# Kernel optimization log

Hardware: AMD Instinct MI355X
Metric: run time of the kernel (lower is better)

The kernel has to match this reference:

```python
import jax, jax.numpy as jnp
import numpy as np

EMBED_DIM = 512
NUM_HEADS = 8
HEAD_DIM = EMBED_DIM // NUM_HEADS
SCALE = HEAD_DIM ** -0.5


def setup_inputs() -> dict:
    key = jax.random.key(0)
    ks = jax.random.split(key, 5)
    B, N, C = 4, 2048, EMBED_DIM
    s = 0.02
    return {
        "x": jax.random.normal(ks[0], (B, N, C), jnp.float32),
        "qkv_w": jax.random.normal(ks[1], (3 * C, C), jnp.float32) * s,
        "qkv_b": jax.random.normal(ks[2], (3 * C,), jnp.float32) * s,
        "proj_w": jax.random.normal(ks[3], (C, C), jnp.float32) * s,
        "proj_b": jax.random.normal(ks[4], (C,), jnp.float32) * s,
    }


def reference(x, qkv_w, qkv_b, proj_w, proj_b):
    B, N, C = x.shape
    H, D = NUM_HEADS, HEAD_DIM
    # qkv: (B, N, 3C) -> (3, B, H, N, D)
    qkv = x @ qkv_w.T + qkv_b
    qkv = qkv.reshape(B, N, 3, H, D).transpose(2, 0, 3, 1, 4)
    q, k, v = qkv[0], qkv[1], qkv[2]
    attn = jnp.einsum("bhnd,bhmd->bhnm", q, k) * SCALE  # (B,H,N,N)
    attn = jax.nn.softmax(attn, axis=-1)
    out = jnp.einsum("bhnm,bhmd->bhnd", attn, v)  # (B,H,N,D)
    out = out.transpose(0, 2, 1, 3).reshape(B, N, C)
    return out @ proj_w.T + proj_b
```

## Files before the change

kernel.cpp:

```cpp
#include <hip/hip_runtime.h>

#define ED 512
#define NH 8
#define HD 64
#define BB 4
#define SEQ 2048
#define MTOT (BB*SEQ)

typedef float f32x4 __attribute__((ext_vector_type(4)));
typedef float f32x16 __attribute__((ext_vector_type(16)));
typedef __bf16 bf16x8 __attribute__((ext_vector_type(8)));
typedef int i32x2 __attribute__((ext_vector_type(2)));
typedef unsigned int u32x4 __attribute__((ext_vector_type(4)));

__device__ __forceinline__ unsigned short f2bf(float f) {
  unsigned int u = __float_as_uint(f);
  u += 0x7FFFu + ((u >> 16) & 1u);
  return (unsigned short)(u >> 16);
}

__device__ __forceinline__ unsigned int cvtpk(float lo, float hi) {
  unsigned int r;
  asm volatile("v_cvt_pk_bf16_f32 %0, %1, %2" : "=v"(r) : "v"(lo), "v"(hi));
  return r;
}

__device__ __forceinline__ void async16(const void* g, void* l) {
  auto gp = (const __attribute__((address_space(1))) unsigned int*)(uintptr_t)(g);
  auto lp = (__attribute__((address_space(3))) unsigned int*)(uintptr_t)(l);
  __builtin_amdgcn_global_load_lds(gp, lp, 16, 0, 0);
}

#define N4_X   1048576
#define N4_WQ  196608
#define N4_WP  65536
__global__ void cvt_all(const float* __restrict__ x,
                        const float* __restrict__ wq_in,
                        const float* __restrict__ wp_in,
                        unsigned short* __restrict__ xb,
                        unsigned short* __restrict__ wq,
                        unsigned short* __restrict__ wp) {
  int i = blockIdx.x * blockDim.x + threadIdx.x;
  const float* src; unsigned short* dst; int off;
  if (i < N4_X)              { src = x;     dst = xb; off = i; }
  else if (i < N4_X + N4_WQ) { src = wq_in; dst = wq; off = i - N4_X; }
  else                       { src = wp_in; dst = wp; off = i - (N4_X + N4_WQ); }
  float4 v = reinterpret_cast<const float4*>(src)[off];
  ushort4 o;
  o.x = f2bf(v.x); o.y = f2bf(v.y); o.z = f2bf(v.z); o.w = f2bf(v.w);
  reinterpret_cast<ushort4*>(dst)[off] = o;
}

template<int MODE, int BM, int NXB>
__global__ __launch_bounds__(256)
void gemm_bt(const unsigned short* __restrict__ A,
             const unsigned short* __restrict__ B,
             const float* __restrict__ bias,
             int M, int N, int K,
             unsigned short* __restrict__ Qo,
             unsigned short* __restrict__ Ko,
             unsigned short* __restrict__ Vo,
             float* __restrict__ Co) {
  __shared__ __align__(16) unsigned short As[2][BM * 64];
  __shared__ __align__(16) unsigned short Bs[2][128 * 64];
  const int FI = BM / 32;
  const int t = threadIdx.x;
  const int l = t & 63;
  const int w = t >> 6;
  const int lo = l & 15, hi = l >> 4;
  const int wr = w >> 1, wc = w & 1;
  const int bid = blockIdx.x;
  const int xcd = bid & 7, idx = bid >> 3;
  const int ypx = (M / BM) >> 3;
  const int m0 = (xcd * ypx + idx / NXB) * BM;
  const int n0 = (idx % NXB) * 128;

  f32x4 acc[FI][4] = {};

  auto stage = [&](int buf, int kt) {
    #pragma unroll
    for (int it = 0; it < BM / 32; ++it) {
      int c = it * 256 + t;
      int row = c >> 3, cin = c & 7;
      int sw = cin ^ (row & 7);
      async16(A + (size_t)(m0 + row) * K + kt * 64 + sw * 8, &As[buf][c * 8]);
    }
    #pragma unroll
    for (int it = 0; it < 4; ++it) {
      int c = it * 256 + t;
      int row = c >> 3, cin = c & 7;
      int sw = cin ^ (row & 7);
      async16(B + (size_t)(n0 + row) * K + kt * 64 + sw * 8, &Bs[buf][c * 8]);
    }
  };

  const int nkt = K >> 6;
  stage(0, 0);
  asm volatile("s_waitcnt vmcnt(0)" ::: "memory");
  __syncthreads();

  for (int kt = 0; kt < nkt; ++kt) {
    const int cur = kt & 1;
    if (kt + 1 < nkt) stage(cur ^ 1, kt + 1);

    __builtin_amdgcn_s_setprio(1);
    #pragma unroll
    for (int kk = 0; kk < 2; ++kk) {
      bf16x8 af[FI], bf[4];
      #pragma unroll
      for (int i = 0; i < FI; ++i) {
        int ra = wr * (BM / 2) + i * 16 + lo;
        int ch = (kk * 4 + hi) ^ (lo & 7);
        af[i] = *reinterpret_cast<const bf16x8*>(&As[cur][ra * 64 + ch * 8]);
      }
      #pragma unroll
      for (int j = 0; j < 4; ++j) {
        int rb = wc * 64 + j * 16 + lo;
        int ch = (kk * 4 + hi) ^ (lo & 7);
        bf[j] = *reinterpret_cast<const bf16x8*>(&Bs[cur][rb * 64 + ch * 8]);
      }
      #pragma unroll
      for (int i = 0; i < FI; ++i)
        #pragma unroll
        for (int j = 0; j < 4; ++j)
          acc[i][j] = __builtin_amdgcn_mfma_f32_16x16x32_bf16(af[i], bf[j], acc[i][j], 0, 0, 0);
    }
    __builtin_amdgcn_s_setprio(0);

    asm volatile("s_waitcnt vmcnt(0)" ::: "memory");
    __syncthreads();
  }

  if (MODE == 0) {
    #pragma unroll
    for (int j = 0; j < 4; ++j) {
      int gcol = n0 + wc * 64 + j * 16 + lo;
      float bv = bias[gcol];
      int which = gcol >> 9;
      int h = (gcol >> 6) & 7;
      int d = gcol & 63;
      #pragma unroll
      for (int i = 0; i < FI; ++i) {
        int rbase = m0 + wr * (BM / 2) + i * 16 + hi * 4;
        int b = rbase >> 11;
        size_t bh = (size_t)(b * NH + h);
        if (which == 2) {
          ushort4 pk;
          pk.x = f2bf(acc[i][j][0] + bv);
          pk.y = f2bf(acc[i][j][1] + bv);
          pk.z = f2bf(acc[i][j][2] + bv);
          pk.w = f2bf(acc[i][j][3] + bv);
          int seq = rbase & 2047;
          *reinterpret_cast<ushort4*>(&Vo[(bh * HD + d) * SEQ + seq]) = pk;
        } else {
          #pragma unroll
          for (int e = 0; e < 4; ++e) {
            int seq = (rbase + e) & 2047;
            float v = acc[i][j][e] + bv;
            if (which == 0)
              Qo[(bh * SEQ + seq) * HD + d] = f2bf(v * 0.18033688f);
            else
              Ko[(bh * SEQ + seq) * HD + d] = f2bf(v);
          }
        }
      }
    }
  } else {
    #pragma unroll
    for (int j = 0; j < 4; ++j) {
      int gcol = n0 + wc * 64 + j * 16 + lo;
      float bv = bias[gcol];
      #pragma unroll
      for (int i = 0; i < FI; ++i) {
        int rbase = m0 + wr * (BM / 2) + i * 16 + hi * 4;
        #pragma unroll
        for (int e = 0; e < 4; ++e)
          Co[(size_t)(rbase + e) * N + gcol] = acc[i][j][e] + bv;
      }
    }
  }
}

__global__ __launch_bounds__(512, 4)
void attn_kernel(const unsigned short* __restrict__ Q,
                 const unsigned short* __restrict__ Kk,
                 const unsigned short* __restrict__ Vt,
                 unsigned short* __restrict__ Ao) {
  __shared__ __align__(16) unsigned short smem[32768];
  auto KsP = [&](int half, int buf) { return &smem[(half * 2 + buf) * 4096]; };
  auto VsP = [&](int half, int buf) { return &smem[16384 + (half * 2 + buf) * 4096]; };
  const int t = threadIdx.x;
  const int l = t & 63;
  const int wid = t >> 6;
  const int qg = wid & 3;
  const int kvh = wid >> 2;
  const int l31 = l & 31, lh = l >> 5;
  const int bid = blockIdx.x;
  const int xcd = bid & 7, idx = bid >> 3;
  const int bh = xcd * 4 + (idx >> 4);
  const int q0 = (idx & 15) * 128;
  const int b = bh >> 3, h = bh & 7;

  bf16x8 qf[4];
  #pragma unroll
  for (int ks = 0; ks < 4; ++ks)
    qf[ks] = *reinterpret_cast<const bf16x8*>(
        &Q[((size_t)bh * SEQ + q0 + qg * 32 + l31) * HD + ks * 16 + lh * 8]);

  f32x16 o0 = {}, o1 = {}, osum = {};
  const __bf16 one1 = (__bf16)1.0f;
  const bf16x8 ones = {one1, one1, one1, one1, one1, one1, one1, one1};

  auto stage = [&](int buf, int kt) {
    const int half = t >> 8;
    const int tt = t & 255;
    const int sbase = half * 1024 + kt * 64;
    unsigned short* kd = KsP(half, buf);
    unsigned short* vd = VsP(half, buf);
    #pragma unroll
    for (int it = 0; it < 2; ++it) {
      int c = it * 256 + tt;
      int row = c >> 3, cin = c & 7;
      int sw = cin ^ (row & 7);
      async16(&Kk[((size_t)bh * SEQ + sbase + row) * HD + sw * 8], kd + c * 8);
    }
    #pragma unroll
    for (int it = 0; it < 2; ++it) {
      int c = it * 256 + tt;
      int row = c >> 3, cin = c & 7;
      int sw = cin ^ (row & 7);
      async16(&Vt[((size_t)bh * HD + row) * SEQ + sbase + sw * 8], vd + c * 8);
    }
  };

  auto tile = [&](int cur, int kt) {
    if (kt + 1 < 16) stage(cur ^ 1, kt + 1);
    const unsigned short* kp = KsP(kvh, cur);
    const unsigned short* vp = VsP(kvh, cur);

    #pragma unroll
    for (int kn = 0; kn < 2; ++kn) {
      f32x16 s = {};
      __builtin_amdgcn_s_setprio(1);
      #pragma unroll
      for (int ks = 0; ks < 4; ++ks) {
        int row = kn * 32 + l31;
        int ch = ((ks * 2 + lh) ^ (l31 & 7)) * 8;
        bf16x8 kf = *reinterpret_cast<const bf16x8*>(&kp[row * 64 + ch]);
        s = __builtin_amdgcn_mfma_f32_32x32x16_bf16(kf, qf[ks], s, 0, 0, 0);
      }
      __builtin_amdgcn_s_setprio(0);

      #pragma unroll
      for (int i = 0; i < 16; ++i) s[i] = __builtin_amdgcn_exp2f(s[i]);

      #pragma unroll
      for (int hs = 0; hs < 2; ++hs) {
        unsigned int w0 = cvtpk(s[8 * hs + 0], s[8 * hs + 1]);
        unsigned int w1 = cvtpk(s[8 * hs + 2], s[8 * hs + 3]);
        unsigned int w2 = cvtpk(s[8 * hs + 4], s[8 * hs + 5]);
        unsigned int w3 = cvtpk(s[8 * hs + 6], s[8 * hs + 7]);
        i32x2 r0 = __builtin_amdgcn_permlane32_swap((int)w0, (int)w2, false, false);
        i32x2 r1 = __builtin_amdgcn_permlane32_swap((int)w1, (int)w3, false, false);
        u32x4 fw = {(unsigned int)r0.x, (unsigned int)r1.x,
                    (unsigned int)r0.y, (unsigned int)r1.y};
        bf16x8 pf = __builtin_bit_cast(bf16x8, fw);

        int ss = kn * 2 + hs;
        int vch = ((ss * 2 + lh) ^ (l31 & 7)) * 8;
        __builtin_amdgcn_s_setprio(1);
        osum = __builtin_amdgcn_mfma_f32_32x32x16_bf16(pf, ones, osum, 0, 0, 0);
        bf16x8 vf0 = *reinterpret_cast<const bf16x8*>(&vp[l31 * 64 + vch]);
        bf16x8 vf1 = *reinterpret_cast<const bf16x8*>(&vp[(32 + l31) * 64 + vch]);
        o0 = __builtin_amdgcn_mfma_f32_32x32x16_bf16(pf, vf0, o0, 0, 0, 0);
        o1 = __builtin_amdgcn_mfma_f32_32x32x16_bf16(pf, vf1, o1, 0, 0, 0);
        __builtin_amdgcn_s_setprio(0);
      }
    }

    asm volatile("s_waitcnt vmcnt(0)" ::: "memory");
    __syncthreads();
  };

  stage(0, 0);
  asm volatile("s_waitcnt vmcnt(0)" ::: "memory");
  __syncthreads();

  for (int k2 = 0; k2 < 8; ++k2) {
    tile(0, 2 * k2);
    tile(1, 2 * k2 + 1);
  }

  float* lds = reinterpret_cast<float*>(&smem[0]);
  const int slot = qg * 64 + l;
  auto coff = [&](int c) {
    return (size_t)slot * 64 + (((c & ~7) | ((c & 7) ^ (l & 7))) << 2);
  };
  if (kvh == 1) {
    #pragma unroll
    for (int c = 0; c < 4; ++c) {
      *reinterpret_cast<f32x4*>(lds + coff(c))     = f32x4{o0[4*c], o0[4*c+1], o0[4*c+2], o0[4*c+3]};
      *reinterpret_cast<f32x4*>(lds + coff(c + 4)) = f32x4{o1[4*c], o1[4*c+1], o1[4*c+2], o1[4*c+3]};
      *reinterpret_cast<f32x4*>(lds + coff(c + 8)) = f32x4{osum[4*c], osum[4*c+1], osum[4*c+2], osum[4*c+3]};
    }
  }
  __syncthreads();
  if (kvh == 0) {
    #pragma unroll
    for (int c = 0; c < 4; ++c) {
      f32x4 a0 = *reinterpret_cast<const f32x4*>(lds + coff(c));
      f32x4 a1 = *reinterpret_cast<const f32x4*>(lds + coff(c + 4));
      f32x4 a2 = *reinterpret_cast<const f32x4*>(lds + coff(c + 8));
      #pragma unroll
      for (int e = 0; e < 4; ++e) {
        o0[4*c+e] += a0[e]; o1[4*c+e] += a1[e]; osum[4*c+e] += a2[e];
      }
    }

    #pragma unroll
    for (int r = 0; r < 16; ++r) {
      int qoff = (r & 3) + 8 * (r >> 2) + 4 * lh;
      int seq = q0 + qg * 32 + qoff;
      float inv = 1.f / osum[r];
      size_t base2 = ((size_t)b * SEQ + seq) * ED + h * HD;
      Ao[base2 + l31]      = f2bf(o0[r] * inv);
      Ao[base2 + 32 + l31] = f2bf(o1[r] * inv);
    }
  }
}

extern "C" void kernel_launch(void* const* d_in, const int* in_sizes, int n_in,
                              void* d_out, int out_size, void* d_ws, size_t ws_size,
                              hipStream_t stream) {
  const float* x      = (const float*)d_in[0];
  const float* qkv_w  = (const float*)d_in[1];
  const float* qkv_b  = (const float*)d_in[2];
  const float* proj_w = (const float*)d_in[3];
  const float* proj_b = (const float*)d_in[4];
  float* out = (float*)d_out;

  char* ws = (char*)d_ws;
  unsigned short* xb = (unsigned short*)(ws);
  unsigned short* wq = (unsigned short*)(ws + 8388608);
  unsigned short* wp = (unsigned short*)(ws + 9961472);
  unsigned short* Q  = (unsigned short*)(ws + 10485760);
  unsigned short* Kb = (unsigned short*)(ws + 18874368);
  unsigned short* Vt = (unsigned short*)(ws + 27262976);
  unsigned short* Ao = (unsigned short*)(ws + 35651584);

  cvt_all<<<(N4_X + N4_WQ + N4_WP + 255) / 256, 256, 0, stream>>>(
      x, qkv_w, proj_w, xb, wq, wp);

  gemm_bt<0, 128, 12><<<768, 256, 0, stream>>>(xb, wq, qkv_b, MTOT, 3 * ED, ED, Q, Kb, Vt, nullptr);

  attn_kernel<<<512, 512, 0, stream>>>(Q, Kb, Vt, Ao);

  gemm_bt<1, 64, 4><<<512, 256, 0, stream>>>(Ao, wp, proj_b, MTOT, ED, ED, nullptr, nullptr, nullptr, out);
}
```

Measured before the change: 82.24 us.

## Fuse fp32-to-bf16 conversion of x into the QKV GEMM A-tile staging

New measurement: 83.63 us. Within noise of the previous version (+1.7%).

```diff
diff --git a/kernel.cpp b/kernel.cpp
--- a/kernel.cpp
+++ b/kernel.cpp
@@ -31,20 +31,16 @@
   __builtin_amdgcn_global_load_lds(gp, lp, 16, 0, 0);
 }
 
-#define N4_X   1048576
 #define N4_WQ  196608
 #define N4_WP  65536
-__global__ void cvt_all(const float* __restrict__ x,
-                        const float* __restrict__ wq_in,
-                        const float* __restrict__ wp_in,
-                        unsigned short* __restrict__ xb,
-                        unsigned short* __restrict__ wq,
-                        unsigned short* __restrict__ wp) {
+__global__ void cvt_w(const float* __restrict__ wq_in,
+                      const float* __restrict__ wp_in,
+                      unsigned short* __restrict__ wq,
+                      unsigned short* __restrict__ wp) {
   int i = blockIdx.x * blockDim.x + threadIdx.x;
   const float* src; unsigned short* dst; int off;
-  if (i < N4_X)              { src = x;     dst = xb; off = i; }
-  else if (i < N4_X + N4_WQ) { src = wq_in; dst = wq; off = i - N4_X; }
-  else                       { src = wp_in; dst = wp; off = i - (N4_X + N4_WQ); }
+  if (i < N4_WQ) { src = wq_in; dst = wq; off = i; }
+  else           { src = wp_in; dst = wp; off = i - N4_WQ; }
   float4 v = reinterpret_cast<const float4*>(src)[off];
   ushort4 o;
   o.x = f2bf(v.x); o.y = f2bf(v.y); o.z = f2bf(v.z); o.w = f2bf(v.w);
@@ -53,7 +49,7 @@
 
 template<int MODE, int BM, int NXB>
 __global__ __launch_bounds__(256)
-void gemm_bt(const unsigned short* __restrict__ A,
+void gemm_bt(const void* __restrict__ Aptr,
              const unsigned short* __restrict__ B,
              const float* __restrict__ bias,
              int M, int N, int K,
@@ -75,16 +71,13 @@
   const int m0 = (xcd * ypx + idx / NXB) * BM;
   const int n0 = (idx % NXB) * 128;
 
+  const float* Af = (const float*)Aptr;
+  const unsigned short* Ab = (const unsigned short*)Aptr;
+
   f32x4 acc[FI][4] = {};
-
-  auto stage = [&](int buf, int kt) {
-    #pragma unroll
-    for (int it = 0; it < BM / 32; ++it) {
-      int c = it * 256 + t;
-      int row = c >> 3, cin = c & 7;
-      int sw = cin ^ (row & 7);
-      async16(A + (size_t)(m0 + row) * K + kt * 64 + sw * 8, &As[buf][c * 8]);
-    }
+  f32x4 alo[FI], ahi[FI];
+
+  auto stageB = [&](int buf, int kt) {
     #pragma unroll
     for (int it = 0; it < 4; ++it) {
       int c = it * 256 + t;
@@ -93,16 +86,40 @@
       async16(B + (size_t)(n0 + row) * K + kt * 64 + sw * 8, &Bs[buf][c * 8]);
     }
   };
-
-  const int nkt = K >> 6;
-  stage(0, 0);
-  asm volatile("s_waitcnt vmcnt(0)" ::: "memory");
-  __syncthreads();
-
-  for (int kt = 0; kt < nkt; ++kt) {
-    const int cur = kt & 1;
-    if (kt + 1 < nkt) stage(cur ^ 1, kt + 1);
-
+  auto stageA_async = [&](int buf, int kt) {
+    #pragma unroll
+    for (int it = 0; it < BM / 32; ++it) {
+      int c = it * 256 + t;
+      int row = c >> 3, cin = c & 7;
+      int sw = cin ^ (row & 7);
+      async16(Ab + (size_t)(m0 + row) * K + kt * 64 + sw * 8, &As[buf][c * 8]);
+    }
+  };
+  auto stageA_load = [&](int kt) {
+    #pragma unroll
+    for (int it = 0; it < BM / 32; ++it) {
+      int c = it * 256 + t;
+      int row = c >> 3, cin = c & 7;
+      int sw = cin ^ (row & 7);
+      const float* src = Af + (size_t)(m0 + row) * K + kt * 64 + sw * 8;
+      alo[it] = *reinterpret_cast<const f32x4*>(src);
+      ahi[it] = *reinterpret_cast<const f32x4*>(src + 4);
+    }
+  };
+  auto stageA_write = [&](int buf) {
+    #pragma unroll
+    for (int it = 0; it < BM / 32; ++it) {
+      int c = it * 256 + t;
+      u32x4 pk;
+      pk[0] = cvtpk(alo[it][0], alo[it][1]);
+      pk[1] = cvtpk(alo[it][2], alo[it][3]);
+      pk[2] = cvtpk(ahi[it][0], ahi[it][1]);
+      pk[3] = cvtpk(ahi[it][2], ahi[it][3]);
+      *reinterpret_cast<u32x4*>(&As[buf][c * 8]) = pk;
+    }
+  };
+
+  auto computeTile = [&](int cur) {
     __builtin_amdgcn_s_setprio(1);
     #pragma unroll
     for (int kk = 0; kk < 2; ++kk) {
@@ -126,9 +143,36 @@
           acc[i][j] = __builtin_amdgcn_mfma_f32_16x16x32_bf16(af[i], bf[j], acc[i][j], 0, 0, 0);
     }
     __builtin_amdgcn_s_setprio(0);
-
+  };
+
+  const int nkt = K >> 6;
+  if (MODE == 0) {
+    stageA_load(0);
+    stageB(0, 0);
+    stageA_write(0);
     asm volatile("s_waitcnt vmcnt(0)" ::: "memory");
     __syncthreads();
+    for (int kt = 0; kt < nkt; ++kt) {
+      const int cur = kt & 1;
+      const bool more = (kt + 1 < nkt);
+      if (more) { stageA_load(kt + 1); stageB(cur ^ 1, kt + 1); }
+      computeTile(cur);
+      if (more) stageA_write(cur ^ 1);
+      asm volatile("s_waitcnt vmcnt(0)" ::: "memory");
+      __syncthreads();
+    }
+  } else {
+    stageA_async(0, 0);
+    stageB(0, 0);
+    asm volatile("s_waitcnt vmcnt(0)" ::: "memory");
+    __syncthreads();
+    for (int kt = 0; kt < nkt; ++kt) {
+      const int cur = kt & 1;
+      if (kt + 1 < nkt) { stageA_async(cur ^ 1, kt + 1); stageB(cur ^ 1, kt + 1); }
+      computeTile(cur);
+      asm volatile("s_waitcnt vmcnt(0)" ::: "memory");
+      __syncthreads();
+    }
   }
 
   if (MODE == 0) {
@@ -340,18 +384,16 @@
   float* out = (float*)d_out;
 
   char* ws = (char*)d_ws;
-  unsigned short* xb = (unsigned short*)(ws);
-  unsigned short* wq = (unsigned short*)(ws + 8388608);
-  unsigned short* wp = (unsigned short*)(ws + 9961472);
-  unsigned short* Q  = (unsigned short*)(ws + 10485760);
-  unsigned short* Kb = (unsigned short*)(ws + 18874368);
-  unsigned short* Vt = (unsigned short*)(ws + 27262976);
-  unsigned short* Ao = (unsigned short*)(ws + 35651584);
-
-  cvt_all<<<(N4_X + N4_WQ + N4_WP + 255) / 256, 256, 0, stream>>>(
-      x, qkv_w, proj_w, xb, wq, wp);
-
-  gemm_bt<0, 128, 12><<<768, 256, 0, stream>>>(xb, wq, qkv_b, MTOT, 3 * ED, ED, Q, Kb, Vt, nullptr);
+  unsigned short* wq = (unsigned short*)(ws);
+  unsigned short* wp = (unsigned short*)(ws + 1572864);
+  unsigned short* Q  = (unsigned short*)(ws + 2097152);
+  unsigned short* Kb = (unsigned short*)(ws + 10485760);
+  unsigned short* Vt = (unsigned short*)(ws + 18874368);
+  unsigned short* Ao = (unsigned short*)(ws + 27262976);
+
+  cvt_w<<<(N4_WQ + N4_WP) / 256, 256, 0, stream>>>(qkv_w, proj_w, wq, wp);
+
+  gemm_bt<0, 64, 12><<<1536, 256, 0, stream>>>(x, wq, qkv_b, MTOT, 3 * ED, ED, Q, Kb, Vt, nullptr);
 
   attn_kernel<<<512, 512, 0, stream>>>(Q, Kb, Vt, Ao);
 
```
